# Kernel optimization log

Measured on AMD Instinct MI355X. Metric: run time of the kernel, lower is better.

The kernel has to match this reference:

```python
import jax, jax.numpy as jnp
import numpy as np

IN_C, OUT_C, K, STRIDE, PAD, N_EXPERTS = 64, 128, 3, 1, 1, 4
B, H, W = 32, 64, 64


def setup_inputs() -> dict:
    key = jax.random.key(0)
    k1, k2, k3, k4 = jax.random.split(key, 4)
    x = jax.random.normal(k1, (B, IN_C, H, W), dtype=jnp.float32)
    idx = jax.random.randint(k2, (B,), 0, N_EXPERTS, dtype=jnp.int64)
    # Expert conv weights/biases (PyTorch Conv2d layout: [out_c, in_c, kh, kw])
    fan_in = IN_C * K * K
    bound = 1.0 / np.sqrt(fan_in)
    Wc = jax.random.uniform(k3, (N_EXPERTS, OUT_C, IN_C, K, K), dtype=jnp.float32,
                            minval=-bound, maxval=bound)
    bc = jax.random.uniform(k4, (N_EXPERTS, OUT_C), dtype=jnp.float32,
                            minval=-bound, maxval=bound)
    return {"x": x, "idx": idx, "Wc": Wc, "bc": bc}


def _conv2d(x, w, b):
    # x: [B, C_in, H, W], w: [C_out, C_in, K, K], b: [C_out]
    y = jax.lax.conv_general_dilated(
        x, w,
        window_strides=(STRIDE, STRIDE),
        padding=[(PAD, PAD), (PAD, PAD)],
        dimension_numbers=("NCHW", "OIHW", "NCHW"),
    )
    return y + b[None, :, None, None]


def reference(x, idx, Wc, bc):
    # Compute every expert's conv for every sample (faithful to the torch code),
    # then gather each sample's selected expert output.
    results = jax.vmap(lambda w, b: _conv2d(x, w, b))(Wc, bc)  # [E, B, C_out, H, W]
    results = jnp.moveaxis(results, 0, 1)                      # [B, E, C_out, H, W]
    out = jnp.take_along_axis(
        results, idx[:, None, None, None, None].astype(jnp.int32), axis=1
    )  # [B, 1, C_out, H, W]
    return jnp.squeeze(out, axis=1)
```

## Files before the change

kernel.cpp:

```cpp
#include <hip/hip_runtime.h>
#include <hip/hip_bf16.h>


#define IC 64
#define OC 128
#define HH 64
#define WW 64

typedef short short8 __attribute__((ext_vector_type(8)));
typedef float float16 __attribute__((ext_vector_type(16)));

static __device__ __forceinline__ ushort f2bf(float v) {
    __hip_bfloat16 h = __float2bfloat16(v);
    return *(ushort*)&h;
}

__global__ __launch_bounds__(256)
void reorder_w(const float* __restrict__ Wc, ushort* __restrict__ wout) {
    const int n = blockIdx.x * 256 + threadIdx.x;
    const float v = Wc[n];
    const int e  = n / 73728;
    int r        = n - e * 73728;
    const int oc = r / 576;
    r           -= oc * 576;
    const int ic  = r / 9;
    const int tap = r - ic * 9;
    wout[((((size_t)e * 9 + tap) * 8 + (ic >> 3)) * 128 + oc) * 8 + (ic & 7)] =
        f2bf(v);
}

__global__ __launch_bounds__(512)
void moe_conv_mfma(const float* __restrict__ x, const int* __restrict__ idx,
                   const ushort* __restrict__ wre, const float* __restrict__ bc,
                   float* __restrict__ out) {
    __shared__ __align__(16) ushort xs[6 * 8 * 66 * 8];
    __shared__ __align__(16) ushort wlds[8192];
    __shared__ float bias[128];

    const int t    = threadIdx.x;
    const int rq   = blockIdx.x;
    const int b    = blockIdx.y;
    const int row0 = rq * 4;
    const int e    = ((unsigned)idx[b]) & 3;

    if (t < 192) {
        const int r = t >> 5, rem = t & 31;
        const int ich = rem >> 2, side = (rem >> 1) & 1, q = rem & 1;
        const int hc = side ? 65 : 0;
        ushort4 z = {0, 0, 0, 0};
        *(ushort4*)&xs[(((r * 8 + ich) * 66 + hc) * 8 + q * 4)] = z;
    } else if (t < 320) {
        bias[t - 192] = bc[e * OC + (t - 192)];
    }

    const float* xb = x + (size_t)b * IC * HH * WW;
    {
        const int gc   = t & 63;
        const int csel = t >> 6;
#pragma unroll
        for (int it = 0; it < 12; ++it) {
            const int combo = it * 8 + csel;
            const int r = combo >> 4, rem = combo & 15;
            const int ich = rem >> 1, q = rem & 1;
            const int gr = row0 - 1 + r;
            ushort4 u = {0, 0, 0, 0};
            if ((unsigned)gr < (unsigned)HH) {
                const int ic0 = ich * 8 + q * 4;
                u.x = f2bf(xb[((ic0 + 0) * HH + gr) * WW + gc]);
                u.y = f2bf(xb[((ic0 + 1) * HH + gr) * WW + gc]);
                u.z = f2bf(xb[((ic0 + 2) * HH + gr) * WW + gc]);
                u.w = f2bf(xb[((ic0 + 3) * HH + gr) * WW + gc]);
            }
            *(ushort4*)&xs[(((r * 8 + ich) * 66 + (gc + 1)) * 8 + q * 4)] = u;
        }
    }

    const int lane31 = t & 31;
    const int lhi    = (t >> 5) & 1;
    const int wv     = t >> 6;
    const int w0     = wv & 1;
    const int pr     = wv >> 1;

    float16 acc[2][2];
#pragma unroll
    for (int a = 0; a < 2; ++a)
#pragma unroll
        for (int cg = 0; cg < 2; ++cg)
#pragma unroll
            for (int r = 0; r < 16; ++r) acc[a][cg][r] = 0.0f;

    const ushort* wsrc = wre + (size_t)e * 9 * 8192;

    uint4 wreg0, wreg1;
    {
        const uint4* g = (const uint4*)wsrc;
        wreg0 = g[t];
        wreg1 = g[512 + t];
    }

    for (int tap = 0; tap < 9; ++tap) {
        __syncthreads();
        *(uint4*)&wlds[(size_t)t * 8]         = wreg0;
        *(uint4*)&wlds[(size_t)(512 + t) * 8] = wreg1;
        __syncthreads();
        if (tap < 8) {
            const uint4* g = (const uint4*)(wsrc + (tap + 1) * 8192);
            wreg0 = g[t];
            wreg1 = g[512 + t];
        }

        const int kh = tap / 3;
        const int kw = tap - kh * 3;
        const int rr = pr + kh;
        const int hb = lane31 + kw;

#pragma unroll
        for (int ks = 0; ks < 4; ++ks) {
            const int ich = ks * 2 + lhi;
            const short8 a0 = *(const short8*)&wlds[(ich * 128 + w0 * 64 + lane31) * 8];
            const short8 a1 = *(const short8*)&wlds[(ich * 128 + w0 * 64 + 32 + lane31) * 8];
            const short8 b0 = *(const short8*)&xs[((rr * 8 + ich) * 66 + hb) * 8];
            const short8 b1 = *(const short8*)&xs[((rr * 8 + ich) * 66 + hb + 32) * 8];
            acc[0][0] = __builtin_amdgcn_mfma_f32_32x32x16_bf16(a0, b0, acc[0][0], 0, 0, 0);
            acc[0][1] = __builtin_amdgcn_mfma_f32_32x32x16_bf16(a0, b1, acc[0][1], 0, 0, 0);
            acc[1][0] = __builtin_amdgcn_mfma_f32_32x32x16_bf16(a1, b0, acc[1][0], 0, 0, 0);
            acc[1][1] = __builtin_amdgcn_mfma_f32_32x32x16_bf16(a1, b1, acc[1][1], 0, 0, 0);
        }
    }

#pragma unroll
    for (int a = 0; a < 2; ++a) {
        const int ocb = w0 * 64 + a * 32 + 4 * lhi;
#pragma unroll
        for (int reg = 0; reg < 16; ++reg) {
            const int oc = ocb + (reg & 3) + 8 * (reg >> 2);
            const float bv = bias[oc];
            const size_t base = (((size_t)b * OC + oc) * HH + (row0 + pr)) * WW;
            out[base + lane31]      = acc[a][0][reg] + bv;
            out[base + 32 + lane31] = acc[a][1][reg] + bv;
        }
    }
}

extern "C" void kernel_launch(void* const* d_in, const int* in_sizes, int n_in,
                              void* d_out, int out_size, void* d_ws, size_t ws_size,
                              hipStream_t stream) {
    const float* x   = (const float*)d_in[0];
    const int*   idx = (const int*)d_in[1];
    const float* Wc  = (const float*)d_in[2];
    const float* bc  = (const float*)d_in[3];
    float* out  = (float*)d_out;
    ushort* wre = (ushort*)d_ws;

    reorder_w<<<1152, 256, 0, stream>>>(Wc, wre);
    dim3 grid(16, 32);
    moe_conv_mfma<<<grid, 512, 0, stream>>>(x, idx, wre, bc, out);
}
```

Measured before the change: 110.6 us.

## Load MFMA weight fragments directly from global, drop weight LDS staging

The conv kernel stops staging each tap's weights through shared memory with two barriers per tap. Instead each lane reads its A-fragment straight from the pre-reordered global weight buffer, prefetching one step ahead across a fully unrolled 36-step loop. The reorder kernel now has each thread gather eight input channels and write one vector store, and the conv kernel gets a launch-bounds occupancy hint. This removes per-tap barriers and the LDS weight traffic, at the cost of more global/L2 weight loads per wave and higher register pressure.

New measurement: 117.7 us. 6.5% more time.

```diff
diff --git a/kernel.cpp b/kernel.cpp
--- a/kernel.cpp
+++ b/kernel.cpp
@@ -8,6 +8,7 @@
 #define WW 64
 
 typedef short short8 __attribute__((ext_vector_type(8)));
+typedef ushort ushort8 __attribute__((ext_vector_type(8)));
 typedef float float16 __attribute__((ext_vector_type(16)));
 
 static __device__ __forceinline__ ushort f2bf(float v) {
@@ -17,24 +18,24 @@
 
 __global__ __launch_bounds__(256)
 void reorder_w(const float* __restrict__ Wc, ushort* __restrict__ wout) {
-    const int n = blockIdx.x * 256 + threadIdx.x;
-    const float v = Wc[n];
-    const int e  = n / 73728;
-    int r        = n - e * 73728;
-    const int oc = r / 576;
-    r           -= oc * 576;
-    const int ic  = r / 9;
-    const int tap = r - ic * 9;
-    wout[((((size_t)e * 9 + tap) * 8 + (ic >> 3)) * 128 + oc) * 8 + (ic & 7)] =
-        f2bf(v);
+    const int u   = blockIdx.x * 256 + threadIdx.x;
+    const int oc  = u & 127;
+    const int ich = (u >> 7) & 7;
+    const int et  = u >> 10;
+    const int tap = et % 9;
+    const int e   = et / 9;
+    const float* src = Wc + (((size_t)(e * 128 + oc) * 64 + ich * 8) * 9 + tap);
+    ushort8 v;
+#pragma unroll
+    for (int j = 0; j < 8; ++j) v[j] = f2bf(src[j * 9]);
+    *(ushort8*)(wout + (size_t)u * 8) = v;
 }
 
-__global__ __launch_bounds__(512)
+__global__ __launch_bounds__(512, 4)
 void moe_conv_mfma(const float* __restrict__ x, const int* __restrict__ idx,
                    const ushort* __restrict__ wre, const float* __restrict__ bc,
                    float* __restrict__ out) {
     __shared__ __align__(16) ushort xs[6 * 8 * 66 * 8];
-    __shared__ __align__(16) ushort wlds[8192];
     __shared__ float bias[128];
 
     const int t    = threadIdx.x;
@@ -42,6 +43,18 @@
     const int b    = blockIdx.y;
     const int row0 = rq * 4;
     const int e    = ((unsigned)idx[b]) & 3;
+
+    const int lane31 = t & 31;
+    const int lhi    = (t >> 5) & 1;
+    const int wv     = t >> 6;
+    const int w0     = wv & 1;
+    const int pr     = wv >> 1;
+
+    const ushort* wsrc = wre + (size_t)e * 9 * 8192
+                       + ((size_t)lhi * 128 + w0 * 64 + lane31) * 8;
+
+    short8 a0c = *(const short8*)(wsrc);
+    short8 a1c = *(const short8*)(wsrc + 256);
 
     if (t < 192) {
         const int r = t >> 5, rem = t & 31;
@@ -75,12 +88,6 @@
         }
     }
 
-    const int lane31 = t & 31;
-    const int lhi    = (t >> 5) & 1;
-    const int wv     = t >> 6;
-    const int w0     = wv & 1;
-    const int pr     = wv >> 1;
-
     float16 acc[2][2];
 #pragma unroll
     for (int a = 0; a < 2; ++a)
@@ -89,43 +96,31 @@
 #pragma unroll
             for (int r = 0; r < 16; ++r) acc[a][cg][r] = 0.0f;
 
-    const ushort* wsrc = wre + (size_t)e * 9 * 8192;
+    __syncthreads();
 
-    uint4 wreg0, wreg1;
-    {
-        const uint4* g = (const uint4*)wsrc;
-        wreg0 = g[t];
-        wreg1 = g[512 + t];
-    }
+    const int xbase = ((pr * 8 + lhi) * 66 + lane31) * 8;
 
-    for (int tap = 0; tap < 9; ++tap) {
-        __syncthreads();
-        *(uint4*)&wlds[(size_t)t * 8]         = wreg0;
-        *(uint4*)&wlds[(size_t)(512 + t) * 8] = wreg1;
-        __syncthreads();
-        if (tap < 8) {
-            const uint4* g = (const uint4*)(wsrc + (tap + 1) * 8192);
-            wreg0 = g[t];
-            wreg1 = g[512 + t];
+#pragma unroll
+    for (int s = 0; s < 36; ++s) {
+        const int tap = s >> 2, ks = s & 3;
+        const int kh  = tap / 3, kw = tap - kh * 3;
+        const int off = ((kh * 8 + ks * 2) * 66 + kw) * 8;
+
+        const short8 b0 = *(const short8*)&xs[xbase + off];
+        const short8 b1 = *(const short8*)&xs[xbase + off + 256];
+
+        short8 a0n, a1n;
+        if (s < 35) {
+            a0n = *(const short8*)(wsrc + (s + 1) * 2048);
+            a1n = *(const short8*)(wsrc + (s + 1) * 2048 + 256);
         }
 
-        const int kh = tap / 3;
-        const int kw = tap - kh * 3;
-        const int rr = pr + kh;
-        const int hb = lane31 + kw;
+        acc[0][0] = __builtin_amdgcn_mfma_f32_32x32x16_bf16(a0c, b0, acc[0][0], 0, 0, 0);
+        acc[0][1] = __builtin_amdgcn_mfma_f32_32x32x16_bf16(a0c, b1, acc[0][1], 0, 0, 0);
+        acc[1][0] = __builtin_amdgcn_mfma_f32_32x32x16_bf16(a1c, b0, acc[1][0], 0, 0, 0);
+        acc[1][1] = __builtin_amdgcn_mfma_f32_32x32x16_bf16(a1c, b1, acc[1][1], 0, 0, 0);
 
-#pragma unroll
-        for (int ks = 0; ks < 4; ++ks) {
-            const int ich = ks * 2 + lhi;
-            const short8 a0 = *(const short8*)&wlds[(ich * 128 + w0 * 64 + lane31) * 8];
-            const short8 a1 = *(const short8*)&wlds[(ich * 128 + w0 * 64 + 32 + lane31) * 8];
-            const short8 b0 = *(const short8*)&xs[((rr * 8 + ich) * 66 + hb) * 8];
-            const short8 b1 = *(const short8*)&xs[((rr * 8 + ich) * 66 + hb + 32) * 8];
-            acc[0][0] = __builtin_amdgcn_mfma_f32_32x32x16_bf16(a0, b0, acc[0][0], 0, 0, 0);
-            acc[0][1] = __builtin_amdgcn_mfma_f32_32x32x16_bf16(a0, b1, acc[0][1], 0, 0, 0);
-            acc[1][0] = __builtin_amdgcn_mfma_f32_32x32x16_bf16(a1, b0, acc[1][0], 0, 0, 0);
-            acc[1][1] = __builtin_amdgcn_mfma_f32_32x32x16_bf16(a1, b1, acc[1][1], 0, 0, 0);
-        }
+        if (s < 35) { a0c = a0n; a1c = a1n; }
     }
 
 #pragma unroll
@@ -152,7 +147,7 @@
     float* out  = (float*)d_out;
     ushort* wre = (ushort*)d_ws;
 
-    reorder_w<<<1152, 256, 0, stream>>>(Wc, wre);
+    reorder_w<<<144, 256, 0, stream>>>(Wc, wre);
     dim3 grid(16, 32);
     moe_conv_mfma<<<grid, 512, 0, stream>>>(x, idx, wre, bc, out);
 }
```
